# Kernel tuning notes

Measured on AMD Instinct MI355X. Metric: run time of the kernel, lower is better.

Reference implementation:

```python
import jax, jax.numpy as jnp
import numpy as np

OUT_H = OUT_W = 7
SAMPLE = 2          # sample_num (sampling_ratio)
SCALE = 0.125       # spatial_scale
IMG = 1600.0        # image size implied by scale * feature size


def setup_inputs() -> dict:
    key = jax.random.key(0)
    k1, k2, k3, k4 = jax.random.split(key, 4)
    N, C, H, W = 2, 256, 200, 200
    K = 1000
    features = jax.random.normal(k1, (N, C, H, W), dtype=jnp.float32)
    b = jax.random.randint(k2, (K,), 0, N).astype(jnp.float32)
    xy = jax.random.uniform(k3, (K, 4), dtype=jnp.float32) * IMG  # raw corners
    x1 = jnp.minimum(xy[:, 0], xy[:, 2]); x2 = jnp.maximum(xy[:, 0], xy[:, 2])
    y1 = jnp.minimum(xy[:, 1], xy[:, 3]); y2 = jnp.maximum(xy[:, 1], xy[:, 3])
    rois = jnp.stack([b, x1, y1, x2, y2], axis=1)  # [K,5]
    return {"features": features, "rois": rois}


def _roi_align(features, rois):
    # Faithful port of torchvision roi_align (aligned=False, sampling_ratio=SAMPLE)
    N, C, H, W = features.shape
    K = rois.shape[0]
    b = rois[:, 0].astype(jnp.int32)
    x1 = rois[:, 1] * SCALE; y1 = rois[:, 2] * SCALE
    x2 = rois[:, 3] * SCALE; y2 = rois[:, 4] * SCALE
    roi_w = jnp.maximum(x2 - x1, 1.0)  # aligned=False forces min size 1
    roi_h = jnp.maximum(y2 - y1, 1.0)
    bin_w = roi_w / OUT_W
    bin_h = roi_h / OUT_H

    # sample coordinates: [K, out*S] along each axis
    pbin = jnp.repeat(jnp.arange(OUT_H, dtype=jnp.float32), SAMPLE)      # bin index
    sub = jnp.tile(jnp.arange(SAMPLE, dtype=jnp.float32) + 0.5, OUT_H)   # sub-sample offset
    ys = y1[:, None] + pbin[None] * bin_h[:, None] + sub[None] * bin_h[:, None] / SAMPLE  # [K,Ny]
    xs = x1[:, None] + pbin[None] * bin_w[:, None] + sub[None] * bin_w[:, None] / SAMPLE  # [K,Nx]

    def axis_terms(c, size):
        valid = (c >= -1.0) & (c <= size)        # torch: zero outside [-1, size]
        c = jnp.maximum(c, 0.0)
        lo0 = jnp.floor(c).astype(jnp.int32)
        hi_edge = lo0 >= size - 1
        lo = jnp.where(hi_edge, size - 1, lo0)
        hi = jnp.where(hi_edge, size - 1, lo0 + 1)
        c = jnp.where(hi_edge, jnp.float32(size - 1), c)
        l = c - lo.astype(jnp.float32)           # fractional part
        return valid, lo, hi, l

    vy, yl, yh, ly = axis_terms(ys, H)
    vx, xl, xh, lx = axis_terms(xs, W)
    hy, hx = 1.0 - ly, 1.0 - lx

    def gather(yi, xi):
        # [K,Ny,Nx,C] gather with per-roi batch index
        return features[b[:, None, None], :, yi[:, :, None], xi[:, None, :]]

    val = (hy[:, :, None] * hx[:, None, :])[..., None] * gather(yl, xl) \
        + (hy[:, :, None] * lx[:, None, :])[..., None] * gather(yl, xh) \
        + (ly[:, :, None] * hx[:, None, :])[..., None] * gather(yh, xl) \
        + (ly[:, :, None] * lx[:, None, :])[..., None] * gather(yh, xh)
    mask = (vy[:, :, None] & vx[:, None, :])[..., None]
    val = jnp.where(mask, val, 0.0)

    # average SAMPLE x SAMPLE points per bin -> [K,C,OUT_H,OUT_W]
    val = val.reshape(K, OUT_H, SAMPLE, OUT_W, SAMPLE, C).mean(axis=(2, 4))
    return val.transpose(0, 3, 1, 2)


def reference(features, rois):
    return _roi_align(features, rois)
```

## Files before the change

### kernel.cpp

```cpp
#include <hip/hip_runtime.h>

constexpr int C = 256, H = 200, W = 200, NB = 2;
constexpr int PH = 7, PW = 7;
constexpr int NS = 14;
constexpr float SCALE = 0.125f;
constexpr int CG = 32, NCG = C / CG;
constexpr int TS = 20;
constexpr int CGF = 8, NGROUPF = C / CGF;

typedef float f32x4 __attribute__((ext_vector_type(4)));

__global__ __launch_bounds__(256) void transpose_kernel(
    const float* __restrict__ feat, ushort* __restrict__ T)
{
    __shared__ float tile[32][36];
    int B = blockIdx.x;
    int xt = B % 7; int tmp = B / 7;
    int y  = tmp % H; tmp /= H;
    int nb = tmp & 1; int cg = tmp >> 1;
    int x0 = xt * 32;
    int xw = min(32, W - x0);

    int t = threadIdx.x;
    {
        int cl = t >> 3, xi = (t & 7) * 4;
        if (xi < xw) {
            const float* src = feat + (((size_t)nb * C + cg * CG + cl) * H + y) * W + x0 + xi;
            float4 v = *reinterpret_cast<const float4*>(src);
            tile[xi + 0][cl] = v.x; tile[xi + 1][cl] = v.y;
            tile[xi + 2][cl] = v.z; tile[xi + 3][cl] = v.w;
        }
    }
    __syncthreads();
    int xl = t >> 3, c4 = (t & 7) * 4;
    if (xl < xw) {
        float4 v = *reinterpret_cast<const float4*>(&tile[xl][c4]);
        uint u0 = __float_as_uint(v.x), u1 = __float_as_uint(v.y);
        uint u2 = __float_as_uint(v.z), u3 = __float_as_uint(v.w);
        u0 = (u0 + 0x7FFFu + ((u0 >> 16) & 1u)) >> 16;
        u1 = (u1 + 0x7FFFu + ((u1 >> 16) & 1u)) >> 16;
        u2 = (u2 + 0x7FFFu + ((u2 >> 16) & 1u)) >> 16;
        u3 = (u3 + 0x7FFFu + ((u3 >> 16) & 1u)) >> 16;
        uint2 o; o.x = u0 | (u1 << 16); o.y = u2 | (u3 << 16);
        ushort* dst = T + ((((size_t)cg * NB + nb) * H + y) * W + (x0 + xl)) * CG + c4;
        *reinterpret_cast<uint2*>(dst) = o;
    }
}

__global__ __launch_bounds__(256) void gather_kernel(
    const ushort* __restrict__ T, const float* __restrict__ rois,
    float* __restrict__ out, int K)
{
    __shared__ int   s_ylo[NS], s_yhi[NS], s_xlo[NS], s_xhi[NS];
    __shared__ float s_wy[NS][2], s_wx[NS][2];
    __shared__ int   s_off[49 * TS];
    __shared__ float s_wgt[49 * TS];
    __shared__ float s_out[CG * 49];

    int B  = blockIdx.x;
    int cg = B & 7;
    int j  = B >> 3;
    int p  = j / K, k = j - p * K;

    const float* r = rois + (size_t)k * 5;
    int b = (int)r[0];
    if (b != p) return;

    float x1 = r[1]*SCALE, y1 = r[2]*SCALE, x2 = r[3]*SCALE, y2 = r[4]*SCALE;
    float bw = fmaxf(x2 - x1, 1.0f) * (1.0f / PW);
    float bh = fmaxf(y2 - y1, 1.0f) * (1.0f / PH);

    int t = threadIdx.x;
    if (t < NS) {
        int ph = t >> 1, s = t & 1;
        float y = y1 + (float)ph * bh + ((float)s + 0.5f) * bh * 0.5f;
        bool v = (y >= -1.0f) && (y <= (float)H);
        float yc = fmaxf(y, 0.0f);
        int lo = (int)yc, hi;
        if (lo >= H - 1) { lo = H - 1; hi = H - 1; yc = (float)(H - 1); }
        else             { hi = lo + 1; }
        float l = yc - (float)lo;
        s_ylo[t] = lo; s_yhi[t] = hi;
        s_wy[t][0] = v ? 1.0f - l : 0.0f;
        s_wy[t][1] = v ? l        : 0.0f;
    } else if (t >= 64 && t < 64 + NS) {
        int i = t - 64, pw = i >> 1, s = i & 1;
        float x = x1 + (float)pw * bw + ((float)s + 0.5f) * bw * 0.5f;
        bool v = (x >= -1.0f) && (x <= (float)W);
        float xc = fmaxf(x, 0.0f);
        int lo = (int)xc, hi;
        if (lo >= W - 1) { lo = W - 1; hi = W - 1; xc = (float)(W - 1); }
        else             { hi = lo + 1; }
        float l = xc - (float)lo;
        s_xlo[i] = lo; s_xhi[i] = hi;
        s_wx[i][0] = v ? 1.0f - l : 0.0f;
        s_wx[i][1] = v ? l        : 0.0f;
    }
    __syncthreads();

    for (int e = t; e < 49 * 16; e += 256) {
        int bin = e >> 4, cr = e & 15;
        int ph = bin / 7, pw = bin - ph * 7;
        int sy = (cr >> 3) & 1, sx = (cr >> 2) & 1, cy = (cr >> 1) & 1, cx = cr & 1;
        int ysi = 2 * ph + sy, xsi = 2 * pw + sx;
        int row = cy ? s_yhi[ysi] : s_ylo[ysi];
        int col = cx ? s_xhi[xsi] : s_xlo[xsi];
        s_off[bin * TS + cr] = (row * W + col) * CG;
        s_wgt[bin * TS + cr] = s_wy[ysi][cy] * s_wx[xsi][cx] * 0.25f;
    }
    __syncthreads();

    if (t < 49 * 4) {
        int bin = t >> 2, q = t & 3;
        const int*   po = s_off + bin * TS;
        const float* pg = s_wgt + bin * TS;
        int4   o0 = *reinterpret_cast<const int4*>(po + 0);
        int4   o1 = *reinterpret_cast<const int4*>(po + 4);
        int4   o2 = *reinterpret_cast<const int4*>(po + 8);
        int4   o3 = *reinterpret_cast<const int4*>(po + 12);
        float4 w0 = *reinterpret_cast<const float4*>(pg + 0);
        float4 w1 = *reinterpret_cast<const float4*>(pg + 4);
        float4 w2 = *reinterpret_cast<const float4*>(pg + 8);
        float4 w3 = *reinterpret_cast<const float4*>(pg + 12);

        const ushort* slab = T + ((size_t)(cg * NB + p) * H * W) * CG + q * 8;
        uint4 d0  = *reinterpret_cast<const uint4*>(slab + o0.x);
        uint4 d1  = *reinterpret_cast<const uint4*>(slab + o0.y);
        uint4 d2  = *reinterpret_cast<const uint4*>(slab + o0.z);
        uint4 d3  = *reinterpret_cast<const uint4*>(slab + o0.w);
        uint4 d4  = *reinterpret_cast<const uint4*>(slab + o1.x);
        uint4 d5  = *reinterpret_cast<const uint4*>(slab + o1.y);
        uint4 d6  = *reinterpret_cast<const uint4*>(slab + o1.z);
        uint4 d7  = *reinterpret_cast<const uint4*>(slab + o1.w);
        uint4 d8  = *reinterpret_cast<const uint4*>(slab + o2.x);
        uint4 d9  = *reinterpret_cast<const uint4*>(slab + o2.y);
        uint4 d10 = *reinterpret_cast<const uint4*>(slab + o2.z);
        uint4 d11 = *reinterpret_cast<const uint4*>(slab + o2.w);
        uint4 d12 = *reinterpret_cast<const uint4*>(slab + o3.x);
        uint4 d13 = *reinterpret_cast<const uint4*>(slab + o3.y);
        uint4 d14 = *reinterpret_cast<const uint4*>(slab + o3.z);
        uint4 d15 = *reinterpret_cast<const uint4*>(slab + o3.w);

        float a0=0,a1=0,a2=0,a3=0,a4=0,a5=0,a6=0,a7=0;
        #define CORNER(dd, ww) \
            a0 += (ww) * __uint_as_float((dd).x << 16);          \
            a1 += (ww) * __uint_as_float((dd).x & 0xFFFF0000u);  \
            a2 += (ww) * __uint_as_float((dd).y << 16);          \
            a3 += (ww) * __uint_as_float((dd).y & 0xFFFF0000u);  \
            a4 += (ww) * __uint_as_float((dd).z << 16);          \
            a5 += (ww) * __uint_as_float((dd).z & 0xFFFF0000u);  \
            a6 += (ww) * __uint_as_float((dd).w << 16);          \
            a7 += (ww) * __uint_as_float((dd).w & 0xFFFF0000u);
        CORNER(d0,  w0.x) CORNER(d1,  w0.y) CORNER(d2,  w0.z) CORNER(d3,  w0.w)
        CORNER(d4,  w1.x) CORNER(d5,  w1.y) CORNER(d6,  w1.z) CORNER(d7,  w1.w)
        CORNER(d8,  w2.x) CORNER(d9,  w2.y) CORNER(d10, w2.z) CORNER(d11, w2.w)
        CORNER(d12, w3.x) CORNER(d13, w3.y) CORNER(d14, w3.z) CORNER(d15, w3.w)
        #undef CORNER

        float* so = s_out + (8 * q) * 49 + bin;
        so[0*49]=a0; so[1*49]=a1; so[2*49]=a2; so[3*49]=a3;
        so[4*49]=a4; so[5*49]=a5; so[6*49]=a6; so[7*49]=a7;
    }
    __syncthreads();

    float* oslab = out + ((size_t)k * C + cg * CG) * (PH * PW);
    for (int i4 = t; i4 < (CG * 49) / 4; i4 += 256) {
        f32x4 v = *reinterpret_cast<const f32x4*>(s_out + 4 * i4);
        __builtin_nontemporal_store(v, reinterpret_cast<f32x4*>(oslab + 4 * i4));
    }
}

struct __attribute__((packed, aligned(4))) f2 { float a, b; };

__global__ __launch_bounds__(256) void roi_align_fallback(
    const float* __restrict__ feat, const float* __restrict__ rois,
    float* __restrict__ out, int K)
{
    __shared__ int   s_ylo[NS], s_yhi[NS];
    __shared__ float s_wy[NS][2];
    __shared__ int   s_xb[NS];
    __shared__ float s_wx[NS][2];

    int B   = blockIdx.x;
    int xcd = B & 7;
    int j   = B >> 3;
    int p   = j / K, k = j - p * K;
    int cb  = (p * 8 + xcd) * CGF;

    const float* r = rois + (size_t)k * 5;
    int   b  = (int)r[0];
    float x1 = r[1]*SCALE, y1 = r[2]*SCALE, x2 = r[3]*SCALE, y2 = r[4]*SCALE;
    float bw = fmaxf(x2 - x1, 1.0f) * (1.0f / PW);
    float bh = fmaxf(y2 - y1, 1.0f) * (1.0f / PH);

    int t = threadIdx.x;
    if (t < NS) {
        int ph = t >> 1, s = t & 1;
        float y = y1 + (float)ph * bh + ((float)s + 0.5f) * bh * 0.5f;
        bool v = (y >= -1.0f) && (y <= (float)H);
        float yc = fmaxf(y, 0.0f);
        int lo = (int)yc, hi;
        if (lo >= H - 1) { lo = H - 1; hi = H - 1; yc = (float)(H - 1); }
        else             { hi = lo + 1; }
        float l = yc - (float)lo;
        s_ylo[t] = lo; s_yhi[t] = hi;
        s_wy[t][0] = v ? 1.0f - l : 0.0f;
        s_wy[t][1] = v ? l        : 0.0f;
    } else if (t >= 64 && t < 64 + NS) {
        int i = t - 64, pw = i >> 1, s = i & 1;
        float x = x1 + (float)pw * bw + ((float)s + 0.5f) * bw * 0.5f;
        bool v = (x >= -1.0f) && (x <= (float)W);
        float xc = fmaxf(x, 0.0f);
        int lo = (int)xc;
        if (lo >= W - 1) {
            s_xb[i] = W - 2; s_wx[i][0] = 0.0f; s_wx[i][1] = v ? 1.0f : 0.0f;
        } else {
            float l = xc - (float)lo;
            s_xb[i] = lo; s_wx[i][0] = v ? 1.0f - l : 0.0f; s_wx[i][1] = v ? l : 0.0f;
        }
    }
    __syncthreads();

    const float* img = feat + (size_t)b * (C * H * W);
    float* out_base = out + ((size_t)k * C + cb) * (PH * PW);

    for (int i = t; i < CGF * PH * PW; i += 256) {
        int cl  = i / (PH * PW);
        int bin = i - cl * (PH * PW);
        int ph  = bin / PW;
        int pw  = bin - ph * PW;
        const float* plane = img + (size_t)(cb + cl) * (H * W);

        float acc = 0.0f;
        #pragma unroll
        for (int sy = 0; sy < 2; ++sy) {
            int ysi = 2 * ph + sy;
            const float* rlo = plane + s_ylo[ysi] * W;
            const float* rhi = plane + s_yhi[ysi] * W;
            float hy = s_wy[ysi][0], ly = s_wy[ysi][1];
            #pragma unroll
            for (int sx = 0; sx < 2; ++sx) {
                int xsi = 2 * pw + sx;
                int xb = s_xb[xsi];
                float w0 = s_wx[xsi][0], w1 = s_wx[xsi][1];
                f2 vlo = *reinterpret_cast<const f2*>(rlo + xb);
                f2 vhi = *reinterpret_cast<const f2*>(rhi + xb);
                acc += hy * (w0 * vlo.a + w1 * vlo.b)
                     + ly * (w0 * vhi.a + w1 * vhi.b);
            }
        }
        __builtin_nontemporal_store(acc * 0.25f, &out_base[i]);
    }
}

extern "C" void kernel_launch(void* const* d_in, const int* in_sizes, int n_in,
                              void* d_out, int out_size, void* d_ws, size_t ws_size,
                              hipStream_t stream) {
    const float* feat = (const float*)d_in[0];
    const float* rois = (const float*)d_in[1];
    float* out = (float*)d_out;
    int K = in_sizes[1] / 5;

    size_t need = (size_t)NCG * NB * H * W * CG * sizeof(ushort);
    if (ws_size >= need) {
        ushort* T = (ushort*)d_ws;
        int tblocks = NCG * NB * H * 7;
        transpose_kernel<<<tblocks, 256, 0, stream>>>(feat, T);
        gather_kernel<<<K * NCG * NB, 256, 0, stream>>>(T, rois, out, K);
    } else {
        roi_align_fallback<<<K * NGROUPF, 256, 0, stream>>>(feat, rois, out, K);
    }
}
```

Baseline: 59.57 us.

## Pipeline per-batch transpose with gather in a merged kernel across three launches

Result: slower. 76.37 us (+28.2%).

```diff
diff --git a/kernel.cpp b/kernel.cpp
--- a/kernel.cpp
+++ b/kernel.cpp
@@ -6,61 +6,69 @@
 constexpr float SCALE = 0.125f;
 constexpr int CG = 32, NCG = C / CG;
 constexpr int TS = 20;
+constexpr int NTP = NCG * H * 7;
 constexpr int CGF = 8, NGROUPF = C / CGF;
 
 typedef float f32x4 __attribute__((ext_vector_type(4)));
-
-__global__ __launch_bounds__(256) void transpose_kernel(
-    const float* __restrict__ feat, ushort* __restrict__ T)
+typedef uint  u32x2 __attribute__((ext_vector_type(2)));
+
+struct GLds {
+    int   ylo[NS], yhi[NS], xlo[NS], xhi[NS];
+    float wy[NS][2], wx[NS][2];
+    int   off[49 * TS];
+    float wgt[49 * TS];
+    float sout[CG * 49];
+};
+struct TLds { float tile[32][36]; };
+
+__global__ __launch_bounds__(256) void work_kernel(
+    const float* __restrict__ feat, const float* __restrict__ rois,
+    ushort* __restrict__ T, float* __restrict__ out,
+    int K, int tp_b, int ntp, int g_b)
 {
-    __shared__ float tile[32][36];
+    __shared__ alignas(16) char lds_raw[sizeof(GLds)];
     int B = blockIdx.x;
-    int xt = B % 7; int tmp = B / 7;
-    int y  = tmp % H; tmp /= H;
-    int nb = tmp & 1; int cg = tmp >> 1;
-    int x0 = xt * 32;
-    int xw = min(32, W - x0);
-
     int t = threadIdx.x;
-    {
-        int cl = t >> 3, xi = (t & 7) * 4;
-        if (xi < xw) {
-            const float* src = feat + (((size_t)nb * C + cg * CG + cl) * H + y) * W + x0 + xi;
-            float4 v = *reinterpret_cast<const float4*>(src);
-            tile[xi + 0][cl] = v.x; tile[xi + 1][cl] = v.y;
-            tile[xi + 2][cl] = v.z; tile[xi + 3][cl] = v.w;
-        }
-    }
-    __syncthreads();
-    int xl = t >> 3, c4 = (t & 7) * 4;
-    if (xl < xw) {
-        float4 v = *reinterpret_cast<const float4*>(&tile[xl][c4]);
-        uint u0 = __float_as_uint(v.x), u1 = __float_as_uint(v.y);
-        uint u2 = __float_as_uint(v.z), u3 = __float_as_uint(v.w);
-        u0 = (u0 + 0x7FFFu + ((u0 >> 16) & 1u)) >> 16;
-        u1 = (u1 + 0x7FFFu + ((u1 >> 16) & 1u)) >> 16;
-        u2 = (u2 + 0x7FFFu + ((u2 >> 16) & 1u)) >> 16;
-        u3 = (u3 + 0x7FFFu + ((u3 >> 16) & 1u)) >> 16;
-        uint2 o; o.x = u0 | (u1 << 16); o.y = u2 | (u3 << 16);
-        ushort* dst = T + ((((size_t)cg * NB + nb) * H + y) * W + (x0 + xl)) * CG + c4;
-        *reinterpret_cast<uint2*>(dst) = o;
-    }
-}
-
-__global__ __launch_bounds__(256) void gather_kernel(
-    const ushort* __restrict__ T, const float* __restrict__ rois,
-    float* __restrict__ out, int K)
-{
-    __shared__ int   s_ylo[NS], s_yhi[NS], s_xlo[NS], s_xhi[NS];
-    __shared__ float s_wy[NS][2], s_wx[NS][2];
-    __shared__ int   s_off[49 * TS];
-    __shared__ float s_wgt[49 * TS];
-    __shared__ float s_out[CG * 49];
-
-    int B  = blockIdx.x;
-    int cg = B & 7;
-    int j  = B >> 3;
-    int p  = j / K, k = j - p * K;
+
+    if (B < ntp) {
+        TLds& L = *reinterpret_cast<TLds*>(lds_raw);
+        int xt = B % 7; int tmp = B / 7;
+        int y  = tmp % H; int cg = tmp / H;
+        int nb = tp_b;
+        int x0 = xt * 32;
+        int xw = min(32, W - x0);
+
+        {
+            int cl = t >> 3, xi = (t & 7) * 4;
+            if (xi < xw) {
+                const float* src = feat + (((size_t)nb * C + cg * CG + cl) * H + y) * W + x0 + xi;
+                float4 v = *reinterpret_cast<const float4*>(src);
+                L.tile[xi + 0][cl] = v.x; L.tile[xi + 1][cl] = v.y;
+                L.tile[xi + 2][cl] = v.z; L.tile[xi + 3][cl] = v.w;
+            }
+        }
+        __syncthreads();
+        int xl = t >> 3, c4 = (t & 7) * 4;
+        if (xl < xw) {
+            float4 v = *reinterpret_cast<const float4*>(&L.tile[xl][c4]);
+            uint u0 = __float_as_uint(v.x), u1 = __float_as_uint(v.y);
+            uint u2 = __float_as_uint(v.z), u3 = __float_as_uint(v.w);
+            u0 = (u0 + 0x7FFFu + ((u0 >> 16) & 1u)) >> 16;
+            u1 = (u1 + 0x7FFFu + ((u1 >> 16) & 1u)) >> 16;
+            u2 = (u2 + 0x7FFFu + ((u2 >> 16) & 1u)) >> 16;
+            u3 = (u3 + 0x7FFFu + ((u3 >> 16) & 1u)) >> 16;
+            u32x2 o; o.x = u0 | (u1 << 16); o.y = u2 | (u3 << 16);
+            ushort* dst = T + ((((size_t)cg * NB + nb) * H + y) * W + (x0 + xl)) * CG + c4;
+            __builtin_nontemporal_store(o, reinterpret_cast<u32x2*>(dst));
+        }
+        return;
+    }
+
+    GLds& L = *reinterpret_cast<GLds*>(lds_raw);
+    int Bg = B - ntp;
+    int cg = Bg & 7;
+    int k  = Bg >> 3;
+    int p  = g_b;
 
     const float* r = rois + (size_t)k * 5;
     int b = (int)r[0];
@@ -70,7 +78,6 @@
     float bw = fmaxf(x2 - x1, 1.0f) * (1.0f / PW);
     float bh = fmaxf(y2 - y1, 1.0f) * (1.0f / PH);
 
-    int t = threadIdx.x;
     if (t < NS) {
         int ph = t >> 1, s = t & 1;
         float y = y1 + (float)ph * bh + ((float)s + 0.5f) * bh * 0.5f;
@@ -80,9 +87,9 @@
         if (lo >= H - 1) { lo = H - 1; hi = H - 1; yc = (float)(H - 1); }
         else             { hi = lo + 1; }
         float l = yc - (float)lo;
-        s_ylo[t] = lo; s_yhi[t] = hi;
-        s_wy[t][0] = v ? 1.0f - l : 0.0f;
-        s_wy[t][1] = v ? l        : 0.0f;
+        L.ylo[t] = lo; L.yhi[t] = hi;
+        L.wy[t][0] = v ? 1.0f - l : 0.0f;
+        L.wy[t][1] = v ? l        : 0.0f;
     } else if (t >= 64 && t < 64 + NS) {
         int i = t - 64, pw = i >> 1, s = i & 1;
         float x = x1 + (float)pw * bw + ((float)s + 0.5f) * bw * 0.5f;
@@ -92,9 +99,9 @@
         if (lo >= W - 1) { lo = W - 1; hi = W - 1; xc = (float)(W - 1); }
         else             { hi = lo + 1; }
         float l = xc - (float)lo;
-        s_xlo[i] = lo; s_xhi[i] = hi;
-        s_wx[i][0] = v ? 1.0f - l : 0.0f;
-        s_wx[i][1] = v ? l        : 0.0f;
+        L.xlo[i] = lo; L.xhi[i] = hi;
+        L.wx[i][0] = v ? 1.0f - l : 0.0f;
+        L.wx[i][1] = v ? l        : 0.0f;
     }
     __syncthreads();
 
@@ -103,17 +110,17 @@
         int ph = bin / 7, pw = bin - ph * 7;
         int sy = (cr >> 3) & 1, sx = (cr >> 2) & 1, cy = (cr >> 1) & 1, cx = cr & 1;
         int ysi = 2 * ph + sy, xsi = 2 * pw + sx;
-        int row = cy ? s_yhi[ysi] : s_ylo[ysi];
-        int col = cx ? s_xhi[xsi] : s_xlo[xsi];
-        s_off[bin * TS + cr] = (row * W + col) * CG;
-        s_wgt[bin * TS + cr] = s_wy[ysi][cy] * s_wx[xsi][cx] * 0.25f;
+        int row = cy ? L.yhi[ysi] : L.ylo[ysi];
+        int col = cx ? L.xhi[xsi] : L.xlo[xsi];
+        L.off[bin * TS + cr] = (row * W + col) * CG;
+        L.wgt[bin * TS + cr] = L.wy[ysi][cy] * L.wx[xsi][cx] * 0.25f;
     }
     __syncthreads();
 
     if (t < 49 * 4) {
         int bin = t >> 2, q = t & 3;
-        const int*   po = s_off + bin * TS;
-        const float* pg = s_wgt + bin * TS;
+        const int*   po = L.off + bin * TS;
+        const float* pg = L.wgt + bin * TS;
         int4   o0 = *reinterpret_cast<const int4*>(po + 0);
         int4   o1 = *reinterpret_cast<const int4*>(po + 4);
         int4   o2 = *reinterpret_cast<const int4*>(po + 8);
@@ -157,7 +164,7 @@
         CORNER(d12, w3.x) CORNER(d13, w3.y) CORNER(d14, w3.z) CORNER(d15, w3.w)
         #undef CORNER
 
-        float* so = s_out + (8 * q) * 49 + bin;
+        float* so = L.sout + (8 * q) * 49 + bin;
         so[0*49]=a0; so[1*49]=a1; so[2*49]=a2; so[3*49]=a3;
         so[4*49]=a4; so[5*49]=a5; so[6*49]=a6; so[7*49]=a7;
     }
@@ -165,7 +172,7 @@
 
     float* oslab = out + ((size_t)k * C + cg * CG) * (PH * PW);
     for (int i4 = t; i4 < (CG * 49) / 4; i4 += 256) {
-        f32x4 v = *reinterpret_cast<const f32x4*>(s_out + 4 * i4);
+        f32x4 v = *reinterpret_cast<const f32x4*>(L.sout + 4 * i4);
         __builtin_nontemporal_store(v, reinterpret_cast<f32x4*>(oslab + 4 * i4));
     }
 }
@@ -264,9 +271,9 @@
     size_t need = (size_t)NCG * NB * H * W * CG * sizeof(ushort);
     if (ws_size >= need) {
         ushort* T = (ushort*)d_ws;
-        int tblocks = NCG * NB * H * 7;
-        transpose_kernel<<<tblocks, 256, 0, stream>>>(feat, T);
-        gather_kernel<<<K * NCG * NB, 256, 0, stream>>>(T, rois, out, K);
+        work_kernel<<<NTP,         256, 0, stream>>>(feat, rois, T, out, K, 0, NTP, -1);
+        work_kernel<<<NTP + K * 8, 256, 0, stream>>>(feat, rois, T, out, K, 1, NTP,  0);
+        work_kernel<<<K * 8,       256, 0, stream>>>(feat, rois, T, out, K, 0,   0,  1);
     } else {
         roi_align_fallback<<<K * NGROUPF, 256, 0, stream>>>(feat, rois, out, K);
     }
```
